# Performance work log

Measured on AMD Instinct MI355X. Metric: run time of the kernel, lower is better.

The kernel has to match this reference:

```python
import jax, jax.numpy as jnp
import numpy as np

D = 2048
H = 16
DFF = 4 * D

def _layernorm(x, scale, bias, eps=1e-5):
    mu = jnp.mean(x, axis=-1, keepdims=True)
    var = jnp.mean(jnp.square(x - mu), axis=-1, keepdims=True)
    return (x - mu) * jax.lax.rsqrt(var + eps) * scale + bias

def setup_inputs() -> dict:
    key = jax.random.key(0)
    ks = jax.random.split(key, 8)
    s = 1.0 / np.sqrt(D)
    x = jax.random.normal(ks[0], (2, 2048, D), dtype=jnp.float32)
    # nn.Linear weights are [out, in]; y = x @ W.T
    wq = jax.random.uniform(ks[1], (D, D), jnp.float32, -s, s)
    wk = jax.random.uniform(ks[2], (D, D), jnp.float32, -s, s)
    wv = jax.random.uniform(ks[3], (D, D), jnp.float32, -s, s)
    wo = jax.random.uniform(ks[4], (D, D), jnp.float32, -s, s)
    w_up = jax.random.uniform(ks[5], (DFF, D), jnp.float32, -s, s)
    w_down = jax.random.uniform(ks[6], (D, DFF), jnp.float32, -1.0 / np.sqrt(DFF), 1.0 / np.sqrt(DFF))
    ln1_w = jnp.ones((D,), jnp.float32); ln1_b = jnp.zeros((D,), jnp.float32)
    ln2_w = jnp.ones((D,), jnp.float32); ln2_b = jnp.zeros((D,), jnp.float32)
    return {"x": x, "wq": wq, "wk": wk, "wv": wv, "wo": wo,
            "w_up": w_up, "w_down": w_down,
            "ln1_w": ln1_w, "ln1_b": ln1_b, "ln2_w": ln2_w, "ln2_b": ln2_b}

def reference(x, wq, wk, wv, wo, w_up, w_down, ln1_w, ln1_b, ln2_w, ln2_b):
    B, S, Dm = x.shape
    hd = Dm // H  # head_dim
    residual = x
    h = _layernorm(x, ln1_w, ln1_b)
    # projections: y = h @ W.T ; reshape to [B, H, S, hd]
    def split_heads(y):
        return y.reshape(B, S, H, hd).transpose(0, 2, 1, 3)
    q = split_heads(h @ wq.T)
    k = split_heads(h @ wk.T)
    v = split_heads(h @ wv.T)
    scores = jnp.einsum('bhqd,bhkd->bhqk', q, k) / np.sqrt(hd).astype(np.float32)
    attn = jax.nn.softmax(scores, axis=-1)
    o = jnp.einsum('bhqk,bhkd->bhqd', attn, v)
    o = o.transpose(0, 2, 1, 3).reshape(B, S, Dm)
    x1 = residual + o @ wo.T  # dropout p=0 -> identity
    h2 = _layernorm(x1, ln2_w, ln2_b)
    ff = jax.nn.relu(h2 @ w_up.T) @ w_down.T
    return x1 + ff
```

## Files before the change

### kernel.cpp

```cpp
#include <hip/hip_runtime.h>


#define D_MODEL 2048
#define N_HEADS 16
#define HEAD_DIM 128
#define DFF_DIM 8192
#define BATCH 2
#define SEQ 2048
#define M_TOK (BATCH*SEQ)

typedef __attribute__((ext_vector_type(8))) __bf16 bf16x8;
typedef __attribute__((ext_vector_type(4))) float f32x4;

struct FalseT { static constexpr bool value = false; };
struct TrueT  { static constexpr bool value = true;  };

__device__ __forceinline__ unsigned short f2bf(float f) {
  union { float f; unsigned u; } v; v.f = f;
  unsigned r = v.u + 0x7fffu + ((v.u >> 16) & 1u);
  return (unsigned short)(r >> 16);
}

__device__ __forceinline__ void gload_lds16(const void* g, void* l) {
  __builtin_amdgcn_global_load_lds(
      (const __attribute__((address_space(1))) unsigned int*)g,
      (__attribute__((address_space(3))) unsigned int*)l, 16, 0, 0);
}

#define BAR __builtin_amdgcn_s_barrier()
#define LG0 asm volatile("s_waitcnt lgkmcnt(0)" ::: "memory")
#define VMW(n) asm volatile("s_waitcnt vmcnt(" #n ")" ::: "memory")
#define PRIO1 __builtin_amdgcn_s_setprio(1)
#define PRIO0 __builtin_amdgcn_s_setprio(0)

__global__ __launch_bounds__(256)
void f2bf_kernel(const float* __restrict__ in, unsigned short* __restrict__ out, long n) {
  long i = ((long)blockIdx.x * 256 + threadIdx.x) * 4;
  if (i < n) {
    float4 v = *(const float4*)&in[i];
    ushort4 r;
    r.x = f2bf(v.x); r.y = f2bf(v.y); r.z = f2bf(v.z); r.w = f2bf(v.w);
    *(ushort4*)&out[i] = r;
  }
}

__global__ __launch_bounds__(256)
void addk_kernel(float* __restrict__ dst, const float* __restrict__ src) {
  long i = ((long)blockIdx.x * 256 + threadIdx.x) * 4;
  float4 d = *(float4*)&dst[i];
  float4 s = *(const float4*)&src[i];
  d.x += s.x; d.y += s.y; d.z += s.z; d.w += s.w;
  *(float4*)&dst[i] = d;
}

__global__ __launch_bounds__(256)
void ln_kernel(const float* __restrict__ x, const float* __restrict__ g,
               const float* __restrict__ b, unsigned short* __restrict__ out) {
  const int row = blockIdx.x, t = threadIdx.x;
  const float* xr = x + (long)row * D_MODEL;
  float4 v0 = *(const float4*)&xr[t * 8];
  float4 v1 = *(const float4*)&xr[t * 8 + 4];
  float s  = v0.x + v0.y + v0.z + v0.w + v1.x + v1.y + v1.z + v1.w;
  float ss = v0.x*v0.x + v0.y*v0.y + v0.z*v0.z + v0.w*v0.w
           + v1.x*v1.x + v1.y*v1.y + v1.z*v1.z + v1.w*v1.w;
  #pragma unroll
  for (int m = 1; m < 64; m <<= 1) { s += __shfl_xor(s, m); ss += __shfl_xor(ss, m); }
  __shared__ float red[8];
  if ((t & 63) == 0) { red[t >> 6] = s; red[4 + (t >> 6)] = ss; }
  __syncthreads();
  s  = red[0] + red[1] + red[2] + red[3];
  ss = red[4] + red[5] + red[6] + red[7];
  const float mu = s * (1.f / D_MODEL);
  const float var = ss * (1.f / D_MODEL) - mu * mu;
  const float rs = rsqrtf(var + 1e-5f);
  float xv[8];
  xv[0]=v0.x; xv[1]=v0.y; xv[2]=v0.z; xv[3]=v0.w; xv[4]=v1.x; xv[5]=v1.y; xv[6]=v1.z; xv[7]=v1.w;
  #pragma unroll
  for (int j = 0; j < 8; j++) {
    int c = t * 8 + j;
    out[(long)row * D_MODEL + c] = f2bf((xv[j] - mu) * rs * g[c] + b[c]);
  }
}

template<int MODE>
__global__ __launch_bounds__(512, 2)
void gemm256(const unsigned short* __restrict__ A, const unsigned short* __restrict__ Bt,
             int N, int Kstride, int Kext,
             const float* __restrict__ resid, float* __restrict__ outf,
             float* __restrict__ pk,
             unsigned short* __restrict__ ob0, unsigned short* __restrict__ ob1,
             unsigned short* __restrict__ ob2) {
  __shared__ __align__(16) char ldsc[131072];
  const int tid = threadIdx.x;
  const int w  = tid >> 6, l = tid & 63;
  const int wm = w >> 2, wn = w & 3;
  const int lr = l & 15, hi = l >> 4;

  const int cpx = (int)gridDim.x >> 3;
  const int tile = ((int)blockIdx.x & 7) * cpx + ((int)blockIdx.x >> 3);
  const int ty = tile & 15;
  const int tx = tile >> 4;
  const long m0 = (long)ty * 256;
  const long n0 = (long)tx * 256;
  const long koff = (long)blockIdx.y * Kext;

  f32x4 acc[8][4] = {};
  bf16x8 a_r[8], b0_r[4], b1_r[4];

  const int trow = tid >> 3;
  const int tcol = ((tid & 7) * 16) ^ ((trow & 7) << 4);
  const char* pA = (const char*)A + ((m0 + trow) * (long)Kstride + koff) * 2 + tcol;
  const char* pB = (const char*)Bt + ((n0 + trow) * (long)Kstride + koff) * 2 + tcol;
  const size_t rowK = (size_t)Kstride * 2;

  auto STGA = [&](int d, int h, int kt) {
    const char* s = pA + (size_t)(h * 128) * rowK + (size_t)kt * 128;
    char* dst = ldsc + d * 32768 + h * 16384 + w * 1024;
    gload_lds16(s, dst);
    gload_lds16(s + 64 * rowK, dst + 8192);
  };
  auto STGB = [&](int d, int h, int kt) {
    const char* s = pB + (size_t)(h * 128) * rowK + (size_t)kt * 128;
    char* dst = ldsc + 65536 + d * 32768 + h * 16384 + w * 1024;
    gload_lds16(s, dst);
    gload_lds16(s + 64 * rowK, dst + 8192);
  };

  const int xor0 = (hi * 16) ^ ((lr & 7) << 4);
  const int xor1 = (64 + hi * 16) ^ ((lr & 7) << 4);
  const char* lA0 = ldsc + wm * 16384 + lr * 128 + xor0;
  const char* lA1 = ldsc + wm * 16384 + lr * 128 + xor1;
  const char* lB0 = ldsc + 65536 + (wn >> 1) * 16384 + (wn & 1) * 8192 + lr * 128 + xor0;
  const char* lB1 = ldsc + 65536 + (wn >> 1) * 16384 + (wn & 1) * 8192 + lr * 128 + xor1;

  auto LDA = [&](int d, int mh) {
    #pragma unroll
    for (int mi = 0; mi < 4; mi++) {
      a_r[mi * 2 + 0] = *(const bf16x8*)(lA0 + d * 32768 + mh * 8192 + mi * 2048);
      a_r[mi * 2 + 1] = *(const bf16x8*)(lA1 + d * 32768 + mh * 8192 + mi * 2048);
    }
  };
  auto LDB = [&](int d, int nh, bf16x8* br) {
    #pragma unroll
    for (int ni = 0; ni < 2; ni++) {
      br[ni * 2 + 0] = *(const bf16x8*)(lB0 + d * 32768 + nh * 4096 + ni * 2048);
      br[ni * 2 + 1] = *(const bf16x8*)(lB1 + d * 32768 + nh * 4096 + ni * 2048);
    }
  };
  auto MF = [&](int mh, int nh, const bf16x8* br) {
    PRIO1;
    #pragma unroll
    for (int mi = 0; mi < 4; mi++)
      #pragma unroll
      for (int ni = 0; ni < 2; ni++) {
        f32x4 c = acc[mh * 4 + mi][nh * 2 + ni];
        c = __builtin_amdgcn_mfma_f32_16x16x32_bf16(a_r[mi * 2 + 0], br[ni * 2 + 0], c, 0, 0, 0);
        c = __builtin_amdgcn_mfma_f32_16x16x32_bf16(a_r[mi * 2 + 1], br[ni * 2 + 1], c, 0, 0, 0);
        acc[mh * 4 + mi][nh * 2 + ni] = c;
      }
    PRIO0;
  };

  STGA(0, 0, 0); STGA(0, 1, 0); STGB(0, 0, 0); STGB(0, 1, 0);
  STGB(1, 0, 1); STGB(1, 1, 1); STGA(1, 0, 1);
  VMW(6); BAR;

  auto iter = [&](int e, auto lastc) {
    constexpr bool L = decltype(lastc)::value;
    LDA(0, 0); LDB(0, 0, b0_r); STGA(1, 1, e + 1);
    BAR; LG0; MF(0, 0, b0_r); BAR;
    LDB(0, 1, b1_r); if constexpr (!L) STGB(0, 0, e + 2);
    BAR; LG0; MF(0, 1, b1_r); BAR;
    LDA(0, 1); if constexpr (!L) STGB(0, 1, e + 2);
    BAR; LG0; MF(1, 0, b0_r); BAR;
    if constexpr (!L) { STGA(0, 0, e + 2); VMW(6); } else { VMW(0); }
    BAR; MF(1, 1, b1_r); BAR;
    LDA(1, 0); LDB(1, 0, b0_r); if constexpr (!L) STGA(0, 1, e + 2);
    BAR; LG0; MF(0, 0, b0_r); BAR;
    LDB(1, 1, b1_r); if constexpr (!L) STGB(1, 0, e + 3);
    BAR; LG0; MF(0, 1, b1_r); BAR;
    LDA(1, 1); if constexpr (!L) STGB(1, 1, e + 3);
    BAR; LG0; MF(1, 0, b0_r); BAR;
    if constexpr (!L) { STGA(1, 0, e + 3); VMW(6); }
    BAR; MF(1, 1, b1_r); BAR;
  };

  const int NITER = Kext >> 7;
  for (int it = 0; it < NITER - 1; it++) iter(2 * it, FalseT{});
  iter(2 * (NITER - 1), TrueT{});

  #pragma unroll
  for (int a = 0; a < 8; a++) {
    const int mh = a >> 2, mi = a & 3;
    #pragma unroll
    for (int bq = 0; bq < 4; bq++) {
      const int nh = bq >> 1, ni = bq & 1;
      long c  = n0 + wn * 64 + nh * 32 + ni * 16 + lr;
      long r0 = m0 + wm * 128 + mh * 64 + mi * 16 + hi * 4;
      if (MODE == 0) {
        int which = (int)(c >> 11);
        int cc = (int)(c & 2047);
        int hh = cc >> 7, dd = cc & 127;
        int bb = (int)(r0 >> 11), sp = (int)(r0 & 2047);
        if (which == 2) {
          ushort4 pkv;
          pkv.x = f2bf(acc[a][bq][0]); pkv.y = f2bf(acc[a][bq][1]);
          pkv.z = f2bf(acc[a][bq][2]); pkv.w = f2bf(acc[a][bq][3]);
          *(ushort4*)&ob2[((long)(bb * N_HEADS + hh) * HEAD_DIM + dd) * SEQ + sp] = pkv;
        } else {
          #pragma unroll
          for (int j = 0; j < 4; j++) {
            long idx = ((long)(bb * N_HEADS + hh) * SEQ + sp + j) * HEAD_DIM + dd;
            unsigned short bv = f2bf(acc[a][bq][j]);
            if (which == 0) ob0[idx] = bv; else ob1[idx] = bv;
          }
        }
      } else if (MODE == 2) {
        #pragma unroll
        for (int j = 0; j < 4; j++)
          ob0[(r0 + j) * (long)N + c] = f2bf(fmaxf(acc[a][bq][j], 0.f));
      } else {
        if (blockIdx.y == 0) {
          #pragma unroll
          for (int j = 0; j < 4; j++) {
            long idx = (r0 + j) * (long)N + c;
            outf[idx] = resid[idx] + acc[a][bq][j];
          }
        } else {
          #pragma unroll
          for (int j = 0; j < 4; j++)
            pk[(r0 + j) * (long)N + c] = acc[a][bq][j];
        }
      }
    }
  }
}

__global__ __launch_bounds__(512)
void attn_kernel(const unsigned short* __restrict__ q, const unsigned short* __restrict__ k,
                 const unsigned short* __restrict__ vt, unsigned short* __restrict__ o) {
  __shared__ __align__(16) unsigned short Kt[2][32 * 128];
  __shared__ __align__(16) unsigned short VT[2][128 * 32];
  __shared__ __align__(16) unsigned short Pl[8][16 * 40];
  const int tid = threadIdx.x, w = tid >> 6, l = tid & 63;
  const int b = blockIdx.z, h = blockIdx.y, qb = blockIdx.x;
  const long base = ((long)(b * N_HEADS + h)) * SEQ * HEAD_DIM;
  const unsigned short* qp = q + base + (long)(qb * 128) * HEAD_DIM;
  const unsigned short* kp = k + base;
  const unsigned short* vp = vt + base;
  const int hi = l >> 4, lr = l & 15;

  bf16x8 qf[4];
  #pragma unroll
  for (int kc = 0; kc < 4; kc++)
    qf[kc] = *(const bf16x8*)&qp[(w * 16 + lr) * HEAD_DIM + kc * 32 + hi * 8];

  f32x4 oacc[8] = {};
  float mrow[4], lsum[4];
  #pragma unroll
  for (int j = 0; j < 4; j++) { mrow[j] = -1e30f; lsum[j] = 0.f; }

  const float sc = 0.08838834764831845f;
  const int NT = SEQ / 32;

  const int krow = w * 4 + hi;
  const long ksrc_off = (long)krow * 256 + (((l & 15) * 16) ^ ((krow & 7) << 4));
  const int vd = w * 16 + (l >> 2);
  const long vsrc_off = (long)vd * (SEQ * 2) + (l & 3) * 16;

  gload_lds16((const char*)kp + ksrc_off, (char*)Kt[0] + w * 1024);
  gload_lds16((const char*)vp + vsrc_off, (char*)VT[0] + w * 1024);

  int cur = 0;
  for (int t = 0; t < NT; t++) {
    if (t < NT - 1) {
      const long k0b = (long)(t + 1) * 64;
      gload_lds16((const char*)kp + (t + 1) * (32 * 256) + ksrc_off, (char*)Kt[cur ^ 1] + w * 1024);
      gload_lds16((const char*)vp + k0b + vsrc_off,                  (char*)VT[cur ^ 1] + w * 1024);
      VMW(2);
    } else {
      VMW(0);
    }
    __builtin_amdgcn_s_barrier();

    const unsigned short* Kc = Kt[cur];
    const unsigned short* Vc = VT[cur];

    f32x4 s[2] = {};
    #pragma unroll
    for (int kt = 0; kt < 2; kt++) {
      int kcol = kt * 16 + lr;
      #pragma unroll
      for (int kc = 0; kc < 4; kc++) {
        int off = (kc * 64 + hi * 16) ^ ((kcol & 7) << 4);
        bf16x8 kf = *(const bf16x8*)((const char*)Kc + kcol * 256 + off);
        s[kt] = __builtin_amdgcn_mfma_f32_16x16x32_bf16(qf[kc], kf, s[kt], 0, 0, 0);
      }
    }
    #pragma unroll
    for (int kt = 0; kt < 2; kt++)
      #pragma unroll
      for (int j = 0; j < 4; j++) s[kt][j] *= sc;

    float pm[4];
    #pragma unroll
    for (int j = 0; j < 4; j++) pm[j] = fmaxf(s[0][j], s[1][j]);
    #pragma unroll
    for (int m = 1; m < 16; m <<= 1)
      #pragma unroll
      for (int j = 0; j < 4; j++) pm[j] = fmaxf(pm[j], __shfl_xor(pm[j], m));
    int need = 0;
    #pragma unroll
    for (int j = 0; j < 4; j++) need |= (pm[j] > mrow[j] + 8.0f);
    if (__any(need)) {
      #pragma unroll
      for (int j = 0; j < 4; j++) {
        float nm = fmaxf(mrow[j], pm[j]);
        float alpha = __expf(mrow[j] - nm);
        mrow[j] = nm;
        lsum[j] *= alpha;
        #pragma unroll
        for (int n = 0; n < 8; n++) oacc[n][j] *= alpha;
      }
    }
    float p0[4], p1[4], ps[4];
    #pragma unroll
    for (int j = 0; j < 4; j++) {
      p0[j] = __expf(s[0][j] - mrow[j]);
      p1[j] = __expf(s[1][j] - mrow[j]);
      ps[j] = p0[j] + p1[j];
    }
    #pragma unroll
    for (int m = 1; m < 16; m <<= 1)
      #pragma unroll
      for (int j = 0; j < 4; j++) ps[j] += __shfl_xor(ps[j], m);
    #pragma unroll
    for (int j = 0; j < 4; j++) lsum[j] += ps[j];

    unsigned short* Pw = Pl[w];
    #pragma unroll
    for (int j = 0; j < 4; j++) {
      int qr = hi * 4 + j;
      Pw[qr * 40 + lr]      = f2bf(p0[j]);
      Pw[qr * 40 + 16 + lr] = f2bf(p1[j]);
    }
    bf16x8 pa = *(const bf16x8*)&Pw[lr * 40 + hi * 8];
    #pragma unroll
    for (int n = 0; n < 8; n++) {
      bf16x8 vf = *(const bf16x8*)&Vc[(n * 16 + lr) * 32 + hi * 8];
      oacc[n] = __builtin_amdgcn_mfma_f32_16x16x32_bf16(pa, vf, oacc[n], 0, 0, 0);
    }
    __builtin_amdgcn_s_barrier();
    cur ^= 1;
  }

  float rls[4];
  #pragma unroll
  for (int j = 0; j < 4; j++) rls[j] = 1.f / lsum[j];
  #pragma unroll
  for (int n = 0; n < 8; n++)
    #pragma unroll
    for (int j = 0; j < 4; j++) {
      int sp = qb * 128 + w * 16 + hi * 4 + j;
      int d = n * 16 + lr;
      o[((long)b * SEQ + sp) * D_MODEL + h * HEAD_DIM + d] = f2bf(oacc[n][j] * rls[j]);
    }
}

extern "C" void kernel_launch(void* const* d_in, const int* in_sizes, int n_in,
                              void* d_out, int out_size, void* d_ws, size_t ws_size,
                              hipStream_t stream) {
  (void)in_sizes; (void)n_in; (void)out_size; (void)ws_size;
  const float* x   = (const float*)d_in[0];
  const float* wq  = (const float*)d_in[1];
  const float* wk  = (const float*)d_in[2];
  const float* wv  = (const float*)d_in[3];
  const float* wo  = (const float*)d_in[4];
  const float* wup = (const float*)d_in[5];
  const float* wdn = (const float*)d_in[6];
  const float* g1  = (const float*)d_in[7];
  const float* b1  = (const float*)d_in[8];
  const float* g2  = (const float*)d_in[9];
  const float* b2  = (const float*)d_in[10];
  float* out = (float*)d_out;

  char* ws = (char*)d_ws;
  size_t off = 0;
  unsigned short* wqkv = (unsigned short*)(ws + off); off += (size_t)3 * D_MODEL * D_MODEL * 2;
  unsigned short* wo_b = (unsigned short*)(ws + off); off += (size_t)D_MODEL * D_MODEL * 2;
  unsigned short* wup_b = (unsigned short*)(ws + off); off += (size_t)DFF_DIM * D_MODEL * 2;
  unsigned short* wdn_b = (unsigned short*)(ws + off); off += (size_t)DFF_DIM * D_MODEL * 2;
  unsigned short* h_b  = (unsigned short*)(ws + off); off += (size_t)M_TOK * D_MODEL * 2;
  unsigned short* q_b  = (unsigned short*)(ws + off); off += (size_t)M_TOK * D_MODEL * 2;
  unsigned short* k_b  = (unsigned short*)(ws + off); off += (size_t)M_TOK * D_MODEL * 2;
  unsigned short* v_b  = (unsigned short*)(ws + off); off += (size_t)M_TOK * D_MODEL * 2;
  unsigned short* ao_b = (unsigned short*)(ws + off); off += (size_t)M_TOK * D_MODEL * 2;
  float* x1            = (float*)(ws + off);          off += (size_t)M_TOK * D_MODEL * 4;
  unsigned short* ffu  = q_b;
  float* PKa = (float*)k_b;
  float* PKd = (float*)wup_b;

  const long nW = (long)D_MODEL * D_MODEL;
  const long nU = (long)DFF_DIM * D_MODEL;
  f2bf_kernel<<<nW / 1024, 256, 0, stream>>>(wq, wqkv, nW);
  f2bf_kernel<<<nW / 1024, 256, 0, stream>>>(wk, wqkv + nW, nW);
  f2bf_kernel<<<nW / 1024, 256, 0, stream>>>(wv, wqkv + 2 * nW, nW);
  f2bf_kernel<<<nW / 1024, 256, 0, stream>>>(wo, wo_b, nW);
  f2bf_kernel<<<nU / 1024, 256, 0, stream>>>(wup, wup_b, nU);
  f2bf_kernel<<<nU / 1024, 256, 0, stream>>>(wdn, wdn_b, nU);

  ln_kernel<<<M_TOK, 256, 0, stream>>>(x, g1, b1, h_b);

  gemm256<0><<<dim3(384, 1), 512, 0, stream>>>(h_b, wqkv, 3 * D_MODEL, D_MODEL, D_MODEL,
                                               nullptr, nullptr, nullptr, q_b, k_b, v_b);

  attn_kernel<<<dim3(SEQ / 128, N_HEADS, BATCH), 512, 0, stream>>>(q_b, k_b, v_b, ao_b);

  gemm256<3><<<dim3(128, 2), 512, 0, stream>>>(ao_b, wo_b, D_MODEL, D_MODEL, D_MODEL / 2,
                                               x, x1, PKa, nullptr, nullptr, nullptr);
  addk_kernel<<<(M_TOK * D_MODEL) / 1024, 256, 0, stream>>>(x1, PKa);

  ln_kernel<<<M_TOK, 256, 0, stream>>>(x1, g2, b2, h_b);

  gemm256<2><<<dim3(512, 1), 512, 0, stream>>>(h_b, wup_b, DFF_DIM, D_MODEL, D_MODEL,
                                               nullptr, nullptr, nullptr, ffu, nullptr, nullptr);

  gemm256<3><<<dim3(128, 2), 512, 0, stream>>>(ffu, wdn_b, D_MODEL, DFF_DIM, DFF_DIM / 2,
                                               x1, out, PKd, nullptr, nullptr, nullptr);
  addk_kernel<<<(M_TOK * D_MODEL) / 1024, 256, 0, stream>>>(out, PKd);
}
```

Measured before the change: 882.0 us.

## Defer softmax row-sum reduction, fold scale into exp, and swizzle V tile in LDS

```diff
diff --git a/kernel.cpp b/kernel.cpp
--- a/kernel.cpp
+++ b/kernel.cpp
@@ -256,17 +256,20 @@
     qf[kc] = *(const bf16x8*)&qp[(w * 16 + lr) * HEAD_DIM + kc * 32 + hi * 8];
 
   f32x4 oacc[8] = {};
-  float mrow[4], lsum[4];
-  #pragma unroll
-  for (int j = 0; j < 4; j++) { mrow[j] = -1e30f; lsum[j] = 0.f; }
+  float mrow[4], msc[4], lsump[4];
+  #pragma unroll
+  for (int j = 0; j < 4; j++) { mrow[j] = -1e30f; msc[j] = -8.8388e28f; lsump[j] = 0.f; }
 
   const float sc = 0.08838834764831845f;
+  const float THRraw = 90.50966799f;
   const int NT = SEQ / 32;
 
   const int krow = w * 4 + hi;
   const long ksrc_off = (long)krow * 256 + (((l & 15) * 16) ^ ((krow & 7) << 4));
   const int vd = w * 16 + (l >> 2);
-  const long vsrc_off = (long)vd * (SEQ * 2) + (l & 3) * 16;
+  const int vslot = (l & 3) ^ ((l >> 3) & 3);
+  const long vsrc_off = (long)vd * (SEQ * 2) + vslot * 16;
+  const int rdslot = hi ^ ((lr >> 1) & 3);
 
   gload_lds16((const char*)kp + ksrc_off, (char*)Kt[0] + w * 1024);
   gload_lds16((const char*)vp + vsrc_off, (char*)VT[0] + w * 1024);
@@ -297,45 +300,36 @@
         s[kt] = __builtin_amdgcn_mfma_f32_16x16x32_bf16(qf[kc], kf, s[kt], 0, 0, 0);
       }
     }
-    #pragma unroll
-    for (int kt = 0; kt < 2; kt++)
+
+    int need = 0;
+    #pragma unroll
+    for (int j = 0; j < 4; j++)
+      need |= (s[0][j] > mrow[j] + THRraw) | (s[1][j] > mrow[j] + THRraw);
+    if (__any(need)) {
+      float pm[4];
       #pragma unroll
-      for (int j = 0; j < 4; j++) s[kt][j] *= sc;
-
-    float pm[4];
-    #pragma unroll
-    for (int j = 0; j < 4; j++) pm[j] = fmaxf(s[0][j], s[1][j]);
-    #pragma unroll
-    for (int m = 1; m < 16; m <<= 1)
+      for (int j = 0; j < 4; j++) pm[j] = fmaxf(s[0][j], s[1][j]);
       #pragma unroll
-      for (int j = 0; j < 4; j++) pm[j] = fmaxf(pm[j], __shfl_xor(pm[j], m));
-    int need = 0;
-    #pragma unroll
-    for (int j = 0; j < 4; j++) need |= (pm[j] > mrow[j] + 8.0f);
-    if (__any(need)) {
+      for (int m = 1; m < 16; m <<= 1)
+        #pragma unroll
+        for (int j = 0; j < 4; j++) pm[j] = fmaxf(pm[j], __shfl_xor(pm[j], m));
       #pragma unroll
       for (int j = 0; j < 4; j++) {
         float nm = fmaxf(mrow[j], pm[j]);
-        float alpha = __expf(mrow[j] - nm);
-        mrow[j] = nm;
-        lsum[j] *= alpha;
+        float alpha = __expf((mrow[j] - nm) * sc);
+        mrow[j] = nm; msc[j] = nm * sc;
+        lsump[j] *= alpha;
         #pragma unroll
         for (int n = 0; n < 8; n++) oacc[n][j] *= alpha;
       }
     }
-    float p0[4], p1[4], ps[4];
+    float p0[4], p1[4];
     #pragma unroll
     for (int j = 0; j < 4; j++) {
-      p0[j] = __expf(s[0][j] - mrow[j]);
-      p1[j] = __expf(s[1][j] - mrow[j]);
-      ps[j] = p0[j] + p1[j];
-    }
-    #pragma unroll
-    for (int m = 1; m < 16; m <<= 1)
-      #pragma unroll
-      for (int j = 0; j < 4; j++) ps[j] += __shfl_xor(ps[j], m);
-    #pragma unroll
-    for (int j = 0; j < 4; j++) lsum[j] += ps[j];
+      p0[j] = __expf(fmaf(s[0][j], sc, -msc[j]));
+      p1[j] = __expf(fmaf(s[1][j], sc, -msc[j]));
+      lsump[j] += p0[j] + p1[j];
+    }
 
     unsigned short* Pw = Pl[w];
     #pragma unroll
@@ -347,16 +341,20 @@
     bf16x8 pa = *(const bf16x8*)&Pw[lr * 40 + hi * 8];
     #pragma unroll
     for (int n = 0; n < 8; n++) {
-      bf16x8 vf = *(const bf16x8*)&Vc[(n * 16 + lr) * 32 + hi * 8];
+      bf16x8 vf = *(const bf16x8*)((const char*)Vc + (n * 16 + lr) * 64 + rdslot * 16);
       oacc[n] = __builtin_amdgcn_mfma_f32_16x16x32_bf16(pa, vf, oacc[n], 0, 0, 0);
     }
     __builtin_amdgcn_s_barrier();
     cur ^= 1;
   }
 
+  #pragma unroll
+  for (int m = 1; m < 16; m <<= 1)
+    #pragma unroll
+    for (int j = 0; j < 4; j++) lsump[j] += __shfl_xor(lsump[j], m);
   float rls[4];
   #pragma unroll
-  for (int j = 0; j < 4; j++) rls[j] = 1.f / lsum[j];
+  for (int j = 0; j < 4; j++) rls[j] = 1.f / lsump[j];
   #pragma unroll
   for (int n = 0; n < 8; n++)
     #pragma unroll
```

Result: faster. 787.8 us (-10.7%).
